# Performance work log

Hardware: AMD Instinct MI355X
Metric: run time of the kernel (lower is better)

The kernel has to match this reference:

```python
import jax, jax.numpy as jnp
import numpy as np

M, N, D, L, DEPTH, WIDTH, BATCH = 64, 4096, 64, 32, 4, 256, 1024
WIN = 2 * L + 1


def setup_inputs() -> dict:
    key = jax.random.key(0)
    ks = jax.random.split(key, 5)
    u = jax.random.normal(ks[0], (BATCH, D), dtype=jnp.float32)
    # xavier-style scaled gaussians for weights, zeros for biases (matches torch init pattern)
    weight0 = jax.random.normal(ks[1], (M, WIDTH, D), dtype=jnp.float32) * (2.0 / (WIDTH + D)) ** 0.5
    bias0 = jnp.zeros((M, WIDTH, 1), dtype=jnp.float32)
    weight = jax.random.normal(ks[2], (DEPTH - 1, M, WIDTH, WIDTH), dtype=jnp.float32) * (1.0 / WIDTH) ** 0.5
    bias = jnp.zeros((DEPTH - 1, M, WIDTH, 1), dtype=jnp.float32)
    weight_final = jax.random.normal(ks[3], (M, WIN, WIDTH), dtype=jnp.float32) * (2.0 / (WIN + WIDTH)) ** 0.5
    bias_final = jnp.zeros((M, WIN, 1), dtype=jnp.float32)
    xi = jax.random.normal(ks[4], (M, N + 2 * L), dtype=jnp.float32) * (2.0 / (M + N + 2 * L)) ** 0.5
    return {"u": u, "weight0": weight0, "bias0": bias0, "weight": weight,
            "bias": bias, "weight_final": weight_final, "bias_final": bias_final, "xi": xi}


def reference(u, weight0, bias0, weight, bias, weight_final, bias_final, xi) -> jnp.ndarray:
    act = jax.nn.sigmoid
    # per-M shared MLP: u1 [M, width, batch]
    u1 = act(jnp.einsum('mwd,bd->mwb', weight0, u) + bias0)
    for i in range(weight.shape[0]):  # small fixed depth loop
        u1 = act(jnp.einsum('mwv,mvb->mwb', weight[i], u1) + bias[i])
    G = act(jnp.einsum('mjw,mwb->mjb', weight_final, u1) + bias_final)
    # sliding-window correlation: out[n, b] = sum_{m,j} xi[m, n+j] * G[m, j, b]
    win = G.shape[1]
    n_out = xi.shape[1] - (win - 1)
    idx = jnp.arange(n_out)[:, None] + jnp.arange(win)[None, :]
    xw = xi[:, idx]
    return jnp.einsum('mnj,mjb->nb', xw, G)  # [N, batch]
```

## Files before the change

### kernel.cpp

```cpp
#include <hip/hip_runtime.h>
#include <math.h>

typedef __attribute__((ext_vector_type(8))) short short8;
typedef __attribute__((ext_vector_type(4))) float floatx4;

__device__ __forceinline__ void load_lds16(const void* g, void* l) {
    __builtin_amdgcn_global_load_lds((const __attribute__((address_space(1))) void*)g,
                                     (__attribute__((address_space(3))) void*)l,
                                     16, 0, 0);
}

__device__ __forceinline__ unsigned short f2bf(float x) {
    union { float f; unsigned int u; } v; v.f = x;
    unsigned int r = v.u + 0x7fffu + ((v.u >> 16) & 1u);
    return (unsigned short)(r >> 16);
}

__device__ __forceinline__ unsigned int pack_bf(float f0, float f1) {
    union { float f; unsigned int u; } a, b;
    a.f = f0; b.f = f1;
    return __builtin_amdgcn_perm(b.u + 0x8000u, a.u + 0x8000u, 0x07060302u);
}

__device__ __forceinline__ float fast_exp2(float x) {
#if __has_builtin(__builtin_amdgcn_exp2f)
    return __builtin_amdgcn_exp2f(x);
#else
    return __expf(x * 0.69314718056f);
#endif
}

__device__ __forceinline__ float fast_rcp(float x) {
#if __has_builtin(__builtin_amdgcn_rcpf)
    return __builtin_amdgcn_rcpf(x);
#else
    return 1.0f / x;
#endif
}

#define NEG_LOG2E (-1.4426950408889634f)

__global__ void prep(const float* __restrict__ w0, const float* __restrict__ w,
                     const float* __restrict__ wf, const float* __restrict__ xi,
                     unsigned short* __restrict__ w0d, unsigned short* __restrict__ wd,
                     unsigned short* __restrict__ wfd, unsigned int* __restrict__ xw) {
    const int bid = blockIdx.x;
    if (bid < 6656) {
        const bool is0 = bid < 512;
        const int c = (is0 ? bid : bid - 512) * 256 + threadIdx.x;
        const int cpm = is0 ? 2048 : 8192;
        const int Kk  = is0 ? 2 : 8;
        const int K   = Kk * 32;
        const int mm  = c / cpm;
        const int cm  = c - mm * cpm;
        const int rblk = cm / (Kk * 64);
        const int rem  = cm - rblk * (Kk * 64);
        const int kk   = rem >> 6;
        const int lane = rem & 63;
        const int r  = rblk * 16 + (lane & 15);
        const int k0 = kk * 32 + (lane >> 4) * 8;
        const float* srcp = (is0 ? w0 : w) + ((size_t)mm * 256 + r) * K + k0;
        unsigned short* dstp = (is0 ? w0d : wd) + (size_t)c * 8;
        float4 a = *(const float4*)srcp;
        float4 b = *(const float4*)(srcp + 4);
        short8 o = { (short)f2bf(a.x), (short)f2bf(a.y), (short)f2bf(a.z), (short)f2bf(a.w),
                     (short)f2bf(b.x), (short)f2bf(b.y), (short)f2bf(b.z), (short)f2bf(b.w) };
        *(short8*)dstp = o;
    } else if (bid < 7680) {
        const int c = (bid - 6656) * 256 + threadIdx.x;
        const int m  = c >> 12;
        const int cm = c & 4095;
        const int rblk = cm >> 9;
        const int rem  = cm & 511;
        const int kk   = rem >> 6;
        const int lane = rem & 63;
        const int r  = rblk * 16 + (lane & 15);
        const int k0 = kk * 32 + (lane >> 4) * 8;
        short8 o = {0,0,0,0,0,0,0,0};
        if (r < 65) {
            const float* srcp = wf + ((size_t)m * 65 + r) * 256 + k0;
            float4 a = *(const float4*)srcp;
            float4 b = *(const float4*)(srcp + 4);
            o = (short8){ (short)f2bf(a.x), (short)f2bf(a.y), (short)f2bf(a.z), (short)f2bf(a.w),
                          (short)f2bf(b.x), (short)f2bf(b.y), (short)f2bf(b.z), (short)f2bf(b.w) };
        }
        *(short8*)(wfd + (size_t)c * 8) = o;
    } else {
        const int n = bid - 7680;
        #pragma unroll
        for (int t = 0; t < 9; ++t) {
            const int idx = t * 256 + threadIdx.x;
            if (idx < 2176) {
                const int m = idx / 34;
                const int pos = idx - m * 34;
                const int j0 = pos * 2;
                const float* xim = xi + (size_t)m * 4160 + n;
                const float v0 = (j0 < 65) ? xim[j0] : 0.0f;
                const float v1 = (j0 + 1 < 65) ? xim[j0 + 1] : 0.0f;
                xw[(size_t)n * 2176 + idx] =
                    (unsigned int)f2bf(v0) | ((unsigned int)f2bf(v1) << 16);
            }
        }
    }
}

template<int K, int I>
__device__ __forceinline__ void load_w(
    const unsigned short* __restrict__ Wt, int wave, int lane, short8 (&w)[I][K / 32])
{
    constexpr int Kk = K / 32;
    const unsigned short* wb = Wt + ((size_t)(wave * I * Kk) * 64 + lane) * 8;
    #pragma unroll
    for (int i = 0; i < I; ++i)
        #pragma unroll
        for (int kk = 0; kk < Kk; ++kk)
            w[i][kk] = *(const short8*)(wb + (size_t)(i * Kk + kk) * 512);
}

template<int K, int I>
__device__ __forceinline__ void mfma_tile(
    const short8 (&w)[I][K / 32], const unsigned short* src, int t,
    int quad, int l16, floatx4 (&acc)[I][4])
{
    constexpr int Kk = K / 32;
    #pragma unroll
    for (int i = 0; i < I; ++i)
        #pragma unroll
        for (int j = 0; j < 4; ++j) acc[i][j] = (floatx4){0.f, 0.f, 0.f, 0.f};
    #pragma unroll
    for (int kk = 0; kk < Kk; ++kk) {
        short8 bf[4];
        #pragma unroll
        for (int j = 0; j < 4; ++j) {
            const int cb = t * 64 + j * 16 + l16;
            bf[j] = *(const short8*)&src[cb * K + (((kk * 4 + quad) ^ (cb & 7)) * 8)];
        }
        #pragma unroll
        for (int i = 0; i < I; ++i)
            #pragma unroll
            for (int j = 0; j < 4; ++j)
                acc[i][j] = __builtin_amdgcn_mfma_f32_16x16x32_bf16(w[i][kk], bf[j], acc[i][j], 0, 0, 0);
    }
}

template<int I>
__device__ __forceinline__ void mlp_write_t(
    const float* __restrict__ bm, unsigned short* dst, int t,
    int wave, int quad, int l16, floatx4 (&acc)[I][4])
{
    const int rbw = wave * (I * 16);
    #pragma unroll
    for (int i = 0; i < I; ++i) {
        const int rb = rbw + i * 16 + quad * 4;
        float c0 = bm[rb]     * NEG_LOG2E;
        float c1 = bm[rb + 1] * NEG_LOG2E;
        float c2 = bm[rb + 2] * NEG_LOG2E;
        float c3 = bm[rb + 3] * NEG_LOG2E;
        #pragma unroll
        for (int j = 0; j < 4; ++j) {
            const int cb = t * 64 + j * 16 + l16;
            float r0 = fast_rcp(1.0f + fast_exp2(fmaf(acc[i][j][0], NEG_LOG2E, c0)));
            float r1 = fast_rcp(1.0f + fast_exp2(fmaf(acc[i][j][1], NEG_LOG2E, c1)));
            float r2 = fast_rcp(1.0f + fast_exp2(fmaf(acc[i][j][2], NEG_LOG2E, c2)));
            float r3 = fast_rcp(1.0f + fast_exp2(fmaf(acc[i][j][3], NEG_LOG2E, c3)));
            uint2 o = { pack_bf(r0, r1), pack_bf(r2, r3) };
            *(uint2*)&dst[cb * 256 + (((rb >> 3) ^ (cb & 7)) * 8) + (rb & 7)] = o;
        }
    }
}

__global__ __launch_bounds__(256, 2)
void fused_mlp(const float* __restrict__ u,
               const unsigned short* __restrict__ w0_bf, const float* __restrict__ b0_,
               const unsigned short* __restrict__ w_bf,  const float* __restrict__ b_,
               const unsigned short* __restrict__ wf_bf, const float* __restrict__ bf_,
               unsigned short* __restrict__ Gflat) {
    __shared__ unsigned short X[128 * 256];

    const int bid = blockIdx.x;
    const int xcd = bid & 7, slot = bid >> 3;
    const int m  = (xcd << 3) + (slot >> 3);
    const int b0 = (slot & 7) << 7;
    const int tid = threadIdx.x, wave = tid >> 6, lane = tid & 63;
    const int quad = lane >> 4, l16 = lane & 15;

    {
        const int b = tid >> 1, hk = tid & 1;
        const float* up = u + (size_t)(b0 + b) * 64 + hk * 32;
        #pragma unroll
        for (int c = 0; c < 4; ++c) {
            float4 v0 = *(const float4*)(up + c * 8);
            float4 v1 = *(const float4*)(up + c * 8 + 4);
            uint4 p = { pack_bf(v0.x, v0.y), pack_bf(v0.z, v0.w),
                        pack_bf(v1.x, v1.y), pack_bf(v1.z, v1.w) };
            *(uint4*)&X[b * 64 + (((hk * 4 + c) ^ (b & 7)) * 8)] = p;
        }
    }
    __syncthreads();

    floatx4 acc[4][4];

    {
        short8 w0r[4][2];
        load_w<64, 4>(w0_bf + (size_t)m * 16384, wave, lane, w0r);
        floatx4 acc2[4][4];
        mfma_tile<64, 4>(w0r, X, 0, quad, l16, acc);
        mfma_tile<64, 4>(w0r, X, 1, quad, l16, acc2);
        __syncthreads();
        mlp_write_t<4>(b0_ + (size_t)m * 256, X, 0, wave, quad, l16, acc);
        mlp_write_t<4>(b0_ + (size_t)m * 256, X, 1, wave, quad, l16, acc2);
        __syncthreads();
    }

    #pragma unroll 1
    for (int l = 0; l < 3; ++l) {
        short8 wr[4][8];
        load_w<256, 4>(w_bf + ((size_t)l * 64 + m) * 65536, wave, lane, wr);
        const float* bm = b_ + ((size_t)l * 64 + m) * 256;
        mfma_tile<256, 4>(wr, X, 0, quad, l16, acc);
        __syncthreads();
        mlp_write_t<4>(bm, X, 0, wave, quad, l16, acc);
        mfma_tile<256, 4>(wr, X, 1, quad, l16, acc);
        __syncthreads();
        mlp_write_t<4>(bm, X, 1, wave, quad, l16, acc);
    }
    __syncthreads();

    {
        short8 wfr[2][8];
        load_w<256, 2>(wf_bf + (size_t)m * 32768, wave, lane, wfr);
        const float* bm = bf_ + (size_t)m * 65;
        unsigned short* Gg = Gflat + (size_t)b0 * 4352 + m * 68;
        floatx4 acf[2][4];
        #pragma unroll
        for (int t = 0; t < 2; ++t) {
            mfma_tile<256, 2>(wfr, X, t, quad, l16, acf);
            #pragma unroll
            for (int i = 0; i < 2; ++i) {
                const int rb = wave * 32 + i * 16 + quad * 4;
                if (rb < 68) {
                    float c[4];
                    #pragma unroll
                    for (int rr = 0; rr < 4; ++rr)
                        c[rr] = (rb + rr < 65) ? bm[rb + rr] * NEG_LOG2E : 0.0f;
                    #pragma unroll
                    for (int j = 0; j < 4; ++j) {
                        const int cb = t * 64 + j * 16 + l16;
                        float r0 = fast_rcp(1.0f + fast_exp2(fmaf(acf[i][j][0], NEG_LOG2E, c[0])));
                        float r1 = fast_rcp(1.0f + fast_exp2(fmaf(acf[i][j][1], NEG_LOG2E, c[1])));
                        float r2 = fast_rcp(1.0f + fast_exp2(fmaf(acf[i][j][2], NEG_LOG2E, c[2])));
                        float r3 = fast_rcp(1.0f + fast_exp2(fmaf(acf[i][j][3], NEG_LOG2E, c[3])));
                        uint2 o = { pack_bf(r0, r1), pack_bf(r2, r3) };
                        *(uint2*)&Gg[(size_t)cb * 4352 + rb] = o;
                    }
                }
            }
        }
    }
}

__global__ __launch_bounds__(256, 3)
void contract_gemm(const unsigned short* __restrict__ XW,
                   const unsigned short* __restrict__ G,
                   float* __restrict__ P) {
    const int bid = blockIdx.x;
    const int xcd = bid & 7, slot = bid >> 3;
    const int kc  = slot >> 5;
    const int rst = slot & 31;
    const int r0 = ((xcd << 2) + (rst >> 3)) << 7;
    const int c0 = (rst & 7) << 7;
    const int kb = kc * 1088;
    float* Pc = P + (size_t)kc * 4096 * 1024;

    __shared__ unsigned short As[128 * 64];
    __shared__ unsigned short Bs[128 * 64];

    const int tid = threadIdx.x;
    const int wave = tid >> 6, lane = tid & 63;
    const int quad = lane >> 4, l16 = lane & 15;
    const int wr = (wave & 1) * 64;
    const int wc = (wave >> 1) * 64;
    const int srow = wave * 32 + (lane >> 3);
    const int spos = lane & 7;

    floatx4 acc[4][4];
    const floatx4 zero = {0.f, 0.f, 0.f, 0.f};
    #pragma unroll
    for (int i = 0; i < 4; ++i)
        #pragma unroll
        for (int j = 0; j < 4; ++j) acc[i][j] = zero;

    for (int k0 = kb; k0 < kb + 1088; k0 += 64) {
        #pragma unroll
        for (int t = 0; t < 4; ++t) {
            const int row = srow + t * 8;
            const int fc  = spos ^ (row & 7);
            load_lds16(XW + (size_t)(r0 + row) * 4352 + k0 + fc * 8,
                       &As[(wave * 32 + t * 8) * 64]);
            load_lds16(G + (size_t)(c0 + row) * 4352 + k0 + fc * 8,
                       &Bs[(wave * 32 + t * 8) * 64]);
        }
        __syncthreads();

        #pragma unroll
        for (int kk = 0; kk < 2; ++kk) {
            short8 af[4], bfr[4];
            #pragma unroll
            for (int i = 0; i < 4; ++i) {
                const int ra = wr + i * 16 + l16;
                af[i]  = *(const short8*)&As[ra * 64 + (((kk * 4 + quad) ^ (ra & 7)) * 8)];
                const int cb = wc + i * 16 + l16;
                bfr[i] = *(const short8*)&Bs[cb * 64 + (((kk * 4 + quad) ^ (cb & 7)) * 8)];
            }
            #pragma unroll
            for (int i = 0; i < 4; ++i)
                #pragma unroll
                for (int j = 0; j < 4; ++j)
                    acc[i][j] = __builtin_amdgcn_mfma_f32_16x16x32_bf16(af[i], bfr[j], acc[i][j], 0, 0, 0);
        }
        __syncthreads();
    }

    #pragma unroll
    for (int i = 0; i < 4; ++i) {
        const int rb = r0 + wr + i * 16 + quad * 4;
        #pragma unroll
        for (int rr = 0; rr < 4; ++rr)
            #pragma unroll
            for (int j = 0; j < 4; ++j) {
                const int col = c0 + wc + j * 16 + l16;
                Pc[(size_t)(rb + rr) * 1024 + col] = acc[i][j][rr];
            }
    }
}

__global__ void reduce4(const float* __restrict__ P, float* __restrict__ out) {
    const int i = blockIdx.x * 256 + threadIdx.x;
    const float4* p = (const float4*)P;
    float4 a = p[i], b = p[i + 1048576], c = p[i + 2097152], d = p[i + 3145728];
    ((float4*)out)[i] = (float4){ a.x + b.x + c.x + d.x, a.y + b.y + c.y + d.y,
                                  a.z + b.z + c.z + d.z, a.w + b.w + c.w + d.w };
}

extern "C" void kernel_launch(void* const* d_in, const int* in_sizes, int n_in,
                              void* d_out, int out_size, void* d_ws, size_t ws_size,
                              hipStream_t stream) {
    const float* u   = (const float*)d_in[0];
    const float* w0  = (const float*)d_in[1];
    const float* b0_ = (const float*)d_in[2];
    const float* w   = (const float*)d_in[3];
    const float* b   = (const float*)d_in[4];
    const float* wf  = (const float*)d_in[5];
    const float* bf_ = (const float*)d_in[6];
    const float* xi  = (const float*)d_in[7];
    float* out = (float*)d_out;

    unsigned short* w0_bf = (unsigned short*)d_ws;
    unsigned short* w_bf  = w0_bf + 1048576;
    unsigned short* wf_bf = w_bf  + 12582912;
    unsigned short* Gflat = wf_bf + 2097152;
    unsigned short* XW    = Gflat + 4456448;
    float*          P     = (float*)(XW + 17825792);

    prep<<<11776, 256, 0, stream>>>(w0, w, wf, xi, w0_bf, w_bf, wf_bf, (unsigned int*)XW);
    fused_mlp<<<512, 256, 0, stream>>>(u, w0_bf, b0_, w_bf, b, wf_bf, bf_, Gflat);
    contract_gemm<<<1024, 256, 0, stream>>>(XW, Gflat, P);
    reduce4<<<4096, 256, 0, stream>>>(P, out);
}
```

Baseline: 220.4 us.

## Pipeline MLP layers in quarter tiles and halve contraction split-K

After: 221.6 us. No clear change (+0.6%).

```diff
diff --git a/kernel.cpp b/kernel.cpp
--- a/kernel.cpp
+++ b/kernel.cpp
@@ -117,6 +117,57 @@
             w[i][kk] = *(const short8*)(wb + (size_t)(i * Kk + kk) * 512);
 }
 
+template<int K>
+__device__ __forceinline__ void mfma_q(
+    const short8 (&w)[4][K / 32], const unsigned short* src, int q,
+    int quad, int l16, floatx4 (&acc)[4][2])
+{
+    constexpr int Kk = K / 32;
+    #pragma unroll
+    for (int i = 0; i < 4; ++i)
+        #pragma unroll
+        for (int j = 0; j < 2; ++j) acc[i][j] = (floatx4){0.f, 0.f, 0.f, 0.f};
+    #pragma unroll
+    for (int kk = 0; kk < Kk; ++kk) {
+        short8 bf[2];
+        #pragma unroll
+        for (int j = 0; j < 2; ++j) {
+            const int cb = q * 32 + j * 16 + l16;
+            bf[j] = *(const short8*)&src[cb * K + (((kk * 4 + quad) ^ (cb & 7)) * 8)];
+        }
+        #pragma unroll
+        for (int i = 0; i < 4; ++i)
+            #pragma unroll
+            for (int j = 0; j < 2; ++j)
+                acc[i][j] = __builtin_amdgcn_mfma_f32_16x16x32_bf16(w[i][kk], bf[j], acc[i][j], 0, 0, 0);
+    }
+}
+
+__device__ __forceinline__ void write_q(
+    const float* __restrict__ bm, unsigned short* dst, int q,
+    int wave, int quad, int l16, floatx4 (&acc)[4][2])
+{
+    const int rbw = wave * 64;
+    #pragma unroll
+    for (int i = 0; i < 4; ++i) {
+        const int rb = rbw + i * 16 + quad * 4;
+        float c0 = bm[rb]     * NEG_LOG2E;
+        float c1 = bm[rb + 1] * NEG_LOG2E;
+        float c2 = bm[rb + 2] * NEG_LOG2E;
+        float c3 = bm[rb + 3] * NEG_LOG2E;
+        #pragma unroll
+        for (int j = 0; j < 2; ++j) {
+            const int cb = q * 32 + j * 16 + l16;
+            float r0 = fast_rcp(1.0f + fast_exp2(fmaf(acc[i][j][0], NEG_LOG2E, c0)));
+            float r1 = fast_rcp(1.0f + fast_exp2(fmaf(acc[i][j][1], NEG_LOG2E, c1)));
+            float r2 = fast_rcp(1.0f + fast_exp2(fmaf(acc[i][j][2], NEG_LOG2E, c2)));
+            float r3 = fast_rcp(1.0f + fast_exp2(fmaf(acc[i][j][3], NEG_LOG2E, c3)));
+            uint2 o = { pack_bf(r0, r1), pack_bf(r2, r3) };
+            *(uint2*)&dst[cb * 256 + (((rb >> 3) ^ (cb & 7)) * 8) + (rb & 7)] = o;
+        }
+    }
+}
+
 template<int K, int I>
 __device__ __forceinline__ void mfma_tile(
     const short8 (&w)[I][K / 32], const unsigned short* src, int t,
@@ -140,32 +191,6 @@
             #pragma unroll
             for (int j = 0; j < 4; ++j)
                 acc[i][j] = __builtin_amdgcn_mfma_f32_16x16x32_bf16(w[i][kk], bf[j], acc[i][j], 0, 0, 0);
-    }
-}
-
-template<int I>
-__device__ __forceinline__ void mlp_write_t(
-    const float* __restrict__ bm, unsigned short* dst, int t,
-    int wave, int quad, int l16, floatx4 (&acc)[I][4])
-{
-    const int rbw = wave * (I * 16);
-    #pragma unroll
-    for (int i = 0; i < I; ++i) {
-        const int rb = rbw + i * 16 + quad * 4;
-        float c0 = bm[rb]     * NEG_LOG2E;
-        float c1 = bm[rb + 1] * NEG_LOG2E;
-        float c2 = bm[rb + 2] * NEG_LOG2E;
-        float c3 = bm[rb + 3] * NEG_LOG2E;
-        #pragma unroll
-        for (int j = 0; j < 4; ++j) {
-            const int cb = t * 64 + j * 16 + l16;
-            float r0 = fast_rcp(1.0f + fast_exp2(fmaf(acc[i][j][0], NEG_LOG2E, c0)));
-            float r1 = fast_rcp(1.0f + fast_exp2(fmaf(acc[i][j][1], NEG_LOG2E, c1)));
-            float r2 = fast_rcp(1.0f + fast_exp2(fmaf(acc[i][j][2], NEG_LOG2E, c2)));
-            float r3 = fast_rcp(1.0f + fast_exp2(fmaf(acc[i][j][3], NEG_LOG2E, c3)));
-            uint2 o = { pack_bf(r0, r1), pack_bf(r2, r3) };
-            *(uint2*)&dst[cb * 256 + (((rb >> 3) ^ (cb & 7)) * 8) + (rb & 7)] = o;
-        }
     }
 }
 
@@ -176,6 +201,7 @@
                const unsigned short* __restrict__ wf_bf, const float* __restrict__ bf_,
                unsigned short* __restrict__ Gflat) {
     __shared__ unsigned short X[128 * 256];
+    __shared__ unsigned short Xin[128 * 64];
 
     const int bid = blockIdx.x;
     const int xcd = bid & 7, slot = bid >> 3;
@@ -193,42 +219,65 @@
             float4 v1 = *(const float4*)(up + c * 8 + 4);
             uint4 p = { pack_bf(v0.x, v0.y), pack_bf(v0.z, v0.w),
                         pack_bf(v1.x, v1.y), pack_bf(v1.z, v1.w) };
-            *(uint4*)&X[b * 64 + (((hk * 4 + c) ^ (b & 7)) * 8)] = p;
-        }
-    }
-    __syncthreads();
-
-    floatx4 acc[4][4];
+            *(uint4*)&Xin[b * 64 + (((hk * 4 + c) ^ (b & 7)) * 8)] = p;
+        }
+    }
+    __syncthreads();
+
+    floatx4 aA[4][2], aB[4][2];
+    short8 wr[4][8];
 
     {
         short8 w0r[4][2];
         load_w<64, 4>(w0_bf + (size_t)m * 16384, wave, lane, w0r);
-        floatx4 acc2[4][4];
-        mfma_tile<64, 4>(w0r, X, 0, quad, l16, acc);
-        mfma_tile<64, 4>(w0r, X, 1, quad, l16, acc2);
-        __syncthreads();
-        mlp_write_t<4>(b0_ + (size_t)m * 256, X, 0, wave, quad, l16, acc);
-        mlp_write_t<4>(b0_ + (size_t)m * 256, X, 1, wave, quad, l16, acc2);
-        __syncthreads();
-    }
-
-    #pragma unroll 1
-    for (int l = 0; l < 3; ++l) {
-        short8 wr[4][8];
-        load_w<256, 4>(w_bf + ((size_t)l * 64 + m) * 65536, wave, lane, wr);
-        const float* bm = b_ + ((size_t)l * 64 + m) * 256;
-        mfma_tile<256, 4>(wr, X, 0, quad, l16, acc);
-        __syncthreads();
-        mlp_write_t<4>(bm, X, 0, wave, quad, l16, acc);
-        mfma_tile<256, 4>(wr, X, 1, quad, l16, acc);
-        __syncthreads();
-        mlp_write_t<4>(bm, X, 1, wave, quad, l16, acc);
-    }
+        const float* bm = b0_ + (size_t)m * 256;
+        mfma_q<64>(w0r, Xin, 0, quad, l16, aA);
+        mfma_q<64>(w0r, Xin, 1, quad, l16, aB); write_q(bm, X, 0, wave, quad, l16, aA);
+        mfma_q<64>(w0r, Xin, 2, quad, l16, aA); write_q(bm, X, 1, wave, quad, l16, aB);
+        load_w<256, 4>(w_bf + (size_t)m * 65536, wave, lane, wr);
+        mfma_q<64>(w0r, Xin, 3, quad, l16, aB); write_q(bm, X, 2, wave, quad, l16, aA);
+        write_q(bm, X, 3, wave, quad, l16, aB);
+    }
+    __syncthreads();
+
+    const float* bm0 = b_ + (size_t)m * 256;
+    const float* bm1 = b_ + ((size_t)64 + m) * 256;
+    const float* bm2 = b_ + ((size_t)128 + m) * 256;
+
+    mfma_q<256>(wr, X, 0, quad, l16, aA);
+    __syncthreads();
+    mfma_q<256>(wr, X, 1, quad, l16, aB); write_q(bm0, X, 0, wave, quad, l16, aA);
+    __syncthreads();
+    mfma_q<256>(wr, X, 2, quad, l16, aA); write_q(bm0, X, 1, wave, quad, l16, aB);
+    __syncthreads();
+    mfma_q<256>(wr, X, 3, quad, l16, aB); write_q(bm0, X, 2, wave, quad, l16, aA);
+    __syncthreads();
+    load_w<256, 4>(w_bf + ((size_t)64 + m) * 65536, wave, lane, wr);
+    write_q(bm0, X, 3, wave, quad, l16, aB);
+    mfma_q<256>(wr, X, 0, quad, l16, aA);
+    __syncthreads();
+    mfma_q<256>(wr, X, 1, quad, l16, aB); write_q(bm1, X, 0, wave, quad, l16, aA);
+    __syncthreads();
+    mfma_q<256>(wr, X, 2, quad, l16, aA); write_q(bm1, X, 1, wave, quad, l16, aB);
+    __syncthreads();
+    mfma_q<256>(wr, X, 3, quad, l16, aB); write_q(bm1, X, 2, wave, quad, l16, aA);
+    __syncthreads();
+    load_w<256, 4>(w_bf + ((size_t)128 + m) * 65536, wave, lane, wr);
+    write_q(bm1, X, 3, wave, quad, l16, aB);
+    mfma_q<256>(wr, X, 0, quad, l16, aA);
+    __syncthreads();
+    mfma_q<256>(wr, X, 1, quad, l16, aB); write_q(bm2, X, 0, wave, quad, l16, aA);
+    __syncthreads();
+    mfma_q<256>(wr, X, 2, quad, l16, aA); write_q(bm2, X, 1, wave, quad, l16, aB);
+    __syncthreads();
+    mfma_q<256>(wr, X, 3, quad, l16, aB); write_q(bm2, X, 2, wave, quad, l16, aA);
+    __syncthreads();
+    short8 wfr[2][8];
+    load_w<256, 2>(wf_bf + (size_t)m * 32768, wave, lane, wfr);
+    write_q(bm2, X, 3, wave, quad, l16, aB);
     __syncthreads();
 
     {
-        short8 wfr[2][8];
-        load_w<256, 2>(wf_bf + (size_t)m * 32768, wave, lane, wfr);
         const float* bm = bf_ + (size_t)m * 65;
         unsigned short* Gg = Gflat + (size_t)b0 * 4352 + m * 68;
         floatx4 acf[2][4];
@@ -269,7 +318,7 @@
     const int rst = slot & 31;
     const int r0 = ((xcd << 2) + (rst >> 3)) << 7;
     const int c0 = (rst & 7) << 7;
-    const int kb = kc * 1088;
+    const int kb = kc * 2176;
     float* Pc = P + (size_t)kc * 4096 * 1024;
 
     __shared__ unsigned short As[128 * 64];
@@ -290,7 +339,7 @@
         #pragma unroll
         for (int j = 0; j < 4; ++j) acc[i][j] = zero;
 
-    for (int k0 = kb; k0 < kb + 1088; k0 += 64) {
+    for (int k0 = kb; k0 < kb + 2176; k0 += 64) {
         #pragma unroll
         for (int t = 0; t < 4; ++t) {
             const int row = srow + t * 8;
@@ -334,12 +383,11 @@
     }
 }
 
-__global__ void reduce4(const float* __restrict__ P, float* __restrict__ out) {
+__global__ void reduce2(const float* __restrict__ P, float* __restrict__ out) {
     const int i = blockIdx.x * 256 + threadIdx.x;
     const float4* p = (const float4*)P;
-    float4 a = p[i], b = p[i + 1048576], c = p[i + 2097152], d = p[i + 3145728];
-    ((float4*)out)[i] = (float4){ a.x + b.x + c.x + d.x, a.y + b.y + c.y + d.y,
-                                  a.z + b.z + c.z + d.z, a.w + b.w + c.w + d.w };
+    float4 a = p[i], b = p[i + 1048576];
+    ((float4*)out)[i] = (float4){ a.x + b.x, a.y + b.y, a.z + b.z, a.w + b.w };
 }
 
 extern "C" void kernel_launch(void* const* d_in, const int* in_sizes, int n_in,
@@ -364,6 +412,6 @@
 
     prep<<<11776, 256, 0, stream>>>(w0, w, wf, xi, w0_bf, w_bf, wf_bf, (unsigned int*)XW);
     fused_mlp<<<512, 256, 0, stream>>>(u, w0_bf, b0_, w_bf, b, wf_bf, bf_, Gflat);
-    contract_gemm<<<1024, 256, 0, stream>>>(XW, Gflat, P);
-    reduce4<<<4096, 256, 0, stream>>>(P, out);
-}
+    contract_gemm<<<512, 256, 0, stream>>>(XW, Gflat, P);
+    reduce2<<<4096, 256, 0, stream>>>(P, out);
+}
```
